# Kernel optimization log

Measured on AMD Instinct MI355X. Metric: run time of the kernel, lower is better.

## Reference

```python
import jax, jax.numpy as jnp
import numpy as np

S, B, D, H = 1024, 8, 256, 8
DH = D // H
N = S * B
E = 262144
EPS = 1e-5


def setup_inputs():
    key = jax.random.key(0)
    ks = jax.random.split(key, 10)
    g = lambda k, shp, s=0.05: jax.random.normal(k, shp, jnp.float32) * s
    return {
        "x": g(ks[0], (S, B, D), 1.0),
        "condition": g(ks[1], (S, B, 1), 1.0),
        "in_proj_w": g(ks[2], (3 * D, D)),
        "in_proj_b": jnp.zeros((3 * D,), jnp.float32),
        "out_proj_w": g(ks[3], (D, D)),
        "out_proj_b": jnp.zeros((D,), jnp.float32),
        "g1": jnp.ones((D,), jnp.float32), "be1": jnp.zeros((D,), jnp.float32),
        "g2": jnp.ones((D,), jnp.float32), "be2": jnp.zeros((D,), jnp.float32),
        "g3": jnp.ones((D,), jnp.float32), "be3": jnp.zeros((D,), jnp.float32),
        "lin_w": g(ks[4], (D, D)),
        "att_src": g(ks[5], (H, DH)),
        "att_dst": g(ks[6], (H, DH)),
        "gat_bias": jnp.zeros((D,), jnp.float32),
        "w1": g(ks[7], (4 * D, D + 1)),
        "bf1": jnp.zeros((4 * D,), jnp.float32),
        "w2": g(ks[8], (D, 4 * D)),
        "bf2": jnp.zeros((D,), jnp.float32),
        "edge_index": jax.random.randint(ks[9], (2, E), 0, N, jnp.int32),
    }


def _ln(x, g, b):
    m = jnp.mean(x, axis=-1, keepdims=True)
    v = jnp.mean((x - m) ** 2, axis=-1, keepdims=True)
    return (x - m) * jax.lax.rsqrt(v + EPS) * g + b


def _forward(x, condition, in_proj_w, in_proj_b, out_proj_w, out_proj_b,
             g1, be1, g2, be2, g3, be3, lin_w, att_src, att_dst, gat_bias,
             w1, bf1, w2, bf2, edge_index):
    # ---- self-attention (torch MHA, seq-major [S,B,D]) ----
    qkv = jnp.einsum('sbd,ed->sbe', x, in_proj_w) + in_proj_b
    q, k, v = jnp.split(qkv, 3, axis=-1)
    q = q.reshape(S, B, H, DH)
    k = k.reshape(S, B, H, DH)
    v = v.reshape(S, B, H, DH)
    scores = jnp.einsum('sbhd,tbhd->bhst', q, k) / np.float32(np.sqrt(DH))
    a = jax.nn.softmax(scores, axis=-1)
    ctx = jnp.einsum('bhst,tbhd->sbhd', a, v).reshape(S, B, D)
    attn_out = ctx @ out_proj_w.T + out_proj_b
    x1 = _ln(x + attn_out, g1, be1)
    # ---- GATConv over flattened (batch-major) nodes ----
    xr = x1.transpose(1, 0, 2).reshape(N, D)          # node i = b*S + s
    xh = (xr @ lin_w.T).reshape(N, H, DH)
    loops = jnp.arange(N, dtype=edge_index.dtype)     # PyG add_self_loops=True
    src = jnp.concatenate([edge_index[0], loops])
    dst = jnp.concatenate([edge_index[1], loops])
    a_src = jnp.sum(xh * att_src, axis=-1)            # [N,H]
    a_dst = jnp.sum(xh * att_dst, axis=-1)
    e = jax.nn.leaky_relu(a_src[src] + a_dst[dst], 0.2)  # [Et,H]
    m = jax.ops.segment_max(e, dst, num_segments=N)
    ee = jnp.exp(e - m[dst])
    z = jax.ops.segment_sum(ee, dst, num_segments=N)
    alpha = ee / z[dst]
    msg = xh[src] * alpha[:, :, None]                 # [Et,H,DH]
    gout = jax.ops.segment_sum(msg, dst, num_segments=N).reshape(N, D) + gat_bias
    gout = gout.reshape(B, S, D).transpose(1, 0, 2)
    x2 = _ln(x1 + gout, g2, be2)
    # ---- conditioned FFN ----
    xc = jnp.concatenate([x2, condition], axis=-1)    # [S,B,D+1]
    h = jax.nn.relu(xc @ w1.T + bf1)
    f = h @ w2.T + bf2
    return _ln(x2 + f, g3, be3)


def reference(x, condition, in_proj_w, in_proj_b, out_proj_w, out_proj_b,
              g1, be1, g2, be2, g3, be3, lin_w, att_src, att_dst, gat_bias,
              w1, bf1, w2, bf2, edge_index):
    return _forward(x, condition, in_proj_w, in_proj_b, out_proj_w, out_proj_b,
                    g1, be1, g2, be2, g3, be3, lin_w, att_src, att_dst, gat_bias,
                    w1, bf1, w2, bf2, edge_index)
```

## Files before the change

### kernel.cpp

```cpp
#include <hip/hip_runtime.h>
#include <hip/hip_bf16.h>

#define S_ 1024
#define B_ 8
#define D_ 256
#define H_ 8
#define DH_ 32
#define N_ 8192
#define E_ 262144
#define ET_ 270336

typedef unsigned short u16;
typedef float f32x4 __attribute__((ext_vector_type(4)));
typedef __bf16 bf16x8 __attribute__((ext_vector_type(8)));
typedef short s16x4 __attribute__((ext_vector_type(4)));

#define QK_SCALE 0.17677669529663687f

__device__ inline u16 f2bf(float v) {
    unsigned int u = __float_as_uint(v);
    u = (u + 0x7fffu + ((u >> 16) & 1u)) >> 16;
    return (u16)u;
}
__device__ inline float bf2f(u16 u) { return __uint_as_float(((unsigned int)u) << 16); }

__device__ inline unsigned int pack_trunc(float lo, float hi) {
    return __builtin_amdgcn_perm(__float_as_uint(hi), __float_as_uint(lo), 0x07060302u);
}

__device__ inline void gload16(const u16* g, u16* l) {
    __builtin_amdgcn_global_load_lds((const __attribute__((address_space(1))) unsigned int*)g,
                                     (__attribute__((address_space(3))) unsigned int*)l, 16, 0, 0);
}

__device__ inline f32x4 mfma16bf(s16x4 a, s16x4 b, f32x4 c) {
#if __has_builtin(__builtin_amdgcn_mfma_f32_16x16x16bf16_1k)
    return __builtin_amdgcn_mfma_f32_16x16x16bf16_1k(a, b, c, 0, 0, 0);
#else
    asm volatile("v_mfma_f32_16x16x16_bf16 %0, %1, %2, %0" : "+v"(c) : "v"(a), "v"(b));
    return c;
#endif
}

__global__ __launch_bounds__(256) void convert_all(const float* __restrict__ x,  const float* __restrict__ wi,
                                                   const float* __restrict__ wo, const float* __restrict__ wl,
                                                   const float* __restrict__ w1, const float* __restrict__ w2,
                                                   u16* __restrict__ Xbf, u16* __restrict__ Wi, u16* __restrict__ Wo,
                                                   u16* __restrict__ Wl, u16* __restrict__ W1, u16* __restrict__ W2,
                                                   int* __restrict__ count, int* __restrict__ cursor)
{
    const int idx = blockIdx.x * 256 + threadIdx.x;
    const int C0 = 524288;
    const int C1 = C0 + 196608;
    const int C2 = C1 + 65536;
    const int C3 = C2 + 65536;
    const int C4 = C3 + 294912;
    const int C5 = C4 + 262144;
    const int C6 = C5 + 16384;
    if (idx < C0) {
        const float4 v = *(const float4*)&x[(size_t)idx * 4];
        u16 o[4] = {f2bf(v.x), f2bf(v.y), f2bf(v.z), f2bf(v.w)};
        *(uint2*)&Xbf[(size_t)idx * 4] = *(uint2*)o;
    }
    else if (idx < C1) { int i = idx - C0; Wi[i] = f2bf(wi[i]); }
    else if (idx < C2) { int i = idx - C1; Wo[i] = f2bf(wo[i]); }
    else if (idx < C3) { int i = idx - C2; Wl[i] = f2bf(wl[i]); }
    else if (idx < C4) { int i = idx - C3; int r = i / 288, k = i - r * 288;
                         W1[i] = (k < 257) ? f2bf(w1[r * 257 + k]) : (u16)0; }
    else if (idx < C5) { int i = idx - C4; W2[i] = f2bf(w2[i]); }
    else if (idx < C6) { int i = idx - C5; if (i < 8192) count[i] = 0; else cursor[i - 8192] = 0; }
}

__global__ __launch_bounds__(256) void gemm_qkv_hist(const u16* __restrict__ A,
                                                     const u16* __restrict__ W,
                                                     const float* __restrict__ bias,
                                                     u16* __restrict__ Cv,
                                                     const int* __restrict__ ei, int* __restrict__ count)
{
    const int tid = threadIdx.x;
    if (blockIdx.x >= 768) {
        const int e = (blockIdx.x - 768) * 256 + tid;
        const int dst = (e < E_) ? ei[E_ + e] : e - E_;
        atomicAdd(&count[dst], 1);
        return;
    }
    __shared__ u16 As[2][128 * 32];
    __shared__ u16 Bs[2][64 * 32];
    const int m0 = (blockIdx.x / 12) * 128, n0 = (blockIdx.x % 12) * 64;
    const int lane = tid & 63, w = tid >> 6;
    const int wm = w >> 1, wn = w & 1;
    const int lr = lane & 15, lg = lane >> 4;

    f32x4 acc[4][2] = {};

    const u16* Ag = A + (size_t)(m0 + (tid >> 2)) * 256 + (tid & 3) * 8;
    const u16* Wg = W + (size_t)(n0 + (tid >> 2)) * 256 + (tid & 3) * 8;

    auto stage = [&](int buf, int k0) {
        gload16(Ag + k0,                    &As[buf][tid * 8]);
        gload16(Ag + (size_t)64 * 256 + k0, &As[buf][64 * 32 + tid * 8]);
        gload16(Wg + k0,                    &Bs[buf][tid * 8]);
    };
    stage(0, 0);
    __syncthreads();
    int cur = 0;
    for (int kt = 0; kt < 8; ++kt) {
        if (kt + 1 < 8) stage(cur ^ 1, (kt + 1) << 5);
        bf16x8 af[4], bg[2];
        #pragma unroll
        for (int i = 0; i < 4; ++i) af[i] = *(const bf16x8*)&As[cur][(wm * 64 + i * 16 + lr) * 32 + lg * 8];
        #pragma unroll
        for (int i = 0; i < 2; ++i) bg[i] = *(const bf16x8*)&Bs[cur][(wn * 32 + i * 16 + lr) * 32 + lg * 8];
        #pragma unroll
        for (int mi = 0; mi < 4; ++mi)
            #pragma unroll
            for (int ni = 0; ni < 2; ++ni)
                acc[mi][ni] = __builtin_amdgcn_mfma_f32_16x16x32_bf16(af[mi], bg[ni], acc[mi][ni], 0, 0, 0);
        __syncthreads();
        cur ^= 1;
    }
    #pragma unroll
    for (int mi = 0; mi < 4; ++mi)
        #pragma unroll
        for (int ni = 0; ni < 2; ++ni) {
            const int col = n0 + wn * 32 + ni * 16 + lr;
            const float bv = bias[col];
            const int part = col >> 8, hh = (col >> 5) & 7, dh = col & 31;
            #pragma unroll
            for (int r = 0; r < 4; ++r) {
                const int row = m0 + wm * 64 + mi * 16 + lg * 4 + r;
                const int ss = row >> 3, bb = row & 7;
                Cv[(((size_t)((part * 8 + bb) * 8 + hh)) * 1024 + ss) * 32 + dh] = f2bf(acc[mi][ni][r] + bv);
            }
        }
}

__global__ __launch_bounds__(512) void attn_mfma(const u16* __restrict__ qkv, u16* __restrict__ ctx,
                                                 const int* __restrict__ count, int* __restrict__ offset)
{
    const int tid = threadIdx.x;
    if (blockIdx.x == 512) {
        __shared__ int s[512];
        const int base = tid * 16;
        int c[16]; int sum = 0;
        #pragma unroll
        for (int i = 0; i < 16; ++i) { c[i] = count[base + i]; sum += c[i]; }
        s[tid] = sum; __syncthreads();
        for (int off = 1; off < 512; off <<= 1) {
            int add = (tid >= off) ? s[tid - off] : 0;
            __syncthreads();
            s[tid] += add;
            __syncthreads();
        }
        int run = (tid == 0) ? 0 : s[tid - 1];
        #pragma unroll
        for (int i = 0; i < 16; ++i) { offset[base + i] = run; run += c[i]; }
        if (tid == 511) offset[8192] = run;
        return;
    }
    const int qt = blockIdx.x & 7, bh = blockIdx.x >> 3;
    const int b = bh >> 3, h = bh & 7;
    const int lane = tid & 63, w = tid >> 6;
    const int c = lane & 15, g = lane >> 4;

    __shared__ __align__(16) u16 Ks[2][128][40];
    __shared__ __align__(16) u16 Vt[2][32][132];

    const size_t plane = (size_t)(b * 8 + h) * 32768;
    const int q0 = qt * 128 + w * 16;
    const bf16x8 qf = *(const bf16x8*)&qkv[plane + (size_t)(q0 + c) * 32 + g * 8];
    const u16* kbase = qkv + 2097152 + plane;

    auto stage = [&](int buf, int kt) {
        const int r = tid >> 2, c0 = (tid & 3) * 8;
        const u16* kp = kbase + (size_t)(kt * 128 + r) * 32 + c0;
        *(uint4*)&Ks[buf][r][c0] = *(const uint4*)kp;
        u16 vb[8];
        *(uint4*)vb = *(const uint4*)(kp + 2097152);
        #pragma unroll
        for (int i = 0; i < 8; ++i) Vt[buf][c0 + i][r] = vb[i];
    };

    float l = 0.f;
    f32x4 o0 = {}, o1 = {};

    stage(0, 0);
    __syncthreads();
    int cur = 0;
    for (int kt = 0; kt < 8; ++kt) {
        if (kt + 1 < 8) stage(cur ^ 1, kt + 1);
        f32x4 sc[8];
        #pragma unroll
        for (int t = 0; t < 8; ++t) {
            const bf16x8 kf = *(const bf16x8*)&Ks[cur][t * 16 + c][g * 8];
            sc[t] = __builtin_amdgcn_mfma_f32_16x16x32_bf16(kf, qf, (f32x4){0.f, 0.f, 0.f, 0.f}, 0, 0, 0);
        }
        unsigned int pb[8][2];
        float ls = 0.f;
        #pragma unroll
        for (int t = 0; t < 8; ++t) {
            const float p0 = __expf(sc[t][0] * QK_SCALE);
            const float p1 = __expf(sc[t][1] * QK_SCALE);
            const float p2 = __expf(sc[t][2] * QK_SCALE);
            const float p3 = __expf(sc[t][3] * QK_SCALE);
            ls += (p0 + p1) + (p2 + p3);
            pb[t][0] = pack_trunc(p0, p1);
            pb[t][1] = pack_trunc(p2, p3);
        }
        l += ls;
        #pragma unroll
        for (int t = 0; t < 8; ++t) {
            union { unsigned int u[2]; s16x4 v; } pu;
            pu.u[0] = pb[t][0]; pu.u[1] = pb[t][1];
            const s16x4 vf0 = *(const s16x4*)&Vt[cur][c][t * 16 + g * 4];
            const s16x4 vf1 = *(const s16x4*)&Vt[cur][16 + c][t * 16 + g * 4];
            o0 = mfma16bf(vf0, pu.v, o0);
            o1 = mfma16bf(vf1, pu.v, o1);
        }
        __syncthreads();
        cur ^= 1;
    }
    l += __shfl_xor(l, 16, 64);
    l += __shfl_xor(l, 32, 64);
    const float inv = 1.f / l;
    u16 ob[8];
    #pragma unroll
    for (int r = 0; r < 4; ++r) { ob[r] = f2bf(o0[r] * inv); ob[4 + r] = f2bf(o1[r] * inv); }
    const size_t obase = ((size_t)(q0 + c) * 8 + b) * 256 + h * 32 + g * 4;
    *(uint2*)&ctx[obase]      = *(uint2*)ob;
    *(uint2*)&ctx[obase + 16] = *(uint2*)(ob + 4);
}

template<int MODE>
__global__ __launch_bounds__(512) void gemm_ln(const u16* __restrict__ A, int lda,
                                               const u16* __restrict__ W, int ldw, int Ksz,
                                               const float* __restrict__ bias,
                                               const float* __restrict__ resid,
                                               const float* __restrict__ gamma,
                                               const float* __restrict__ beta,
                                               const float* __restrict__ att_s,
                                               const float* __restrict__ att_d,
                                               float* __restrict__ outf,
                                               u16* __restrict__ outn,
                                               float* __restrict__ asrc,
                                               float* __restrict__ adst,
                                               const int* __restrict__ ei,
                                               const int* __restrict__ offset,
                                               int* __restrict__ cursor,
                                               int* __restrict__ sorted)
{
    constexpr int BM = 32;
    const int tid = threadIdx.x;
    if (MODE == 0 && blockIdx.x >= 256) {
        const int e = (blockIdx.x - 256) * 512 + tid;
        int src, dst;
        if (e < E_) { src = ei[e]; dst = ei[E_ + e]; }
        else        { src = dst = e - E_; }
        const int pos = offset[dst] + atomicAdd(&cursor[dst], 1);
        sorted[pos] = src;
        return;
    }
    __shared__ u16 As[2][BM * 32];
    __shared__ u16 Bs[2][256 * 32];
    __shared__ float2 red[BM][8];
    const int m0 = blockIdx.x * BM;
    const int lane = tid & 63, w = tid >> 6;
    const int rw = w >> 2, cw = w & 3;
    const int lr = lane & 15, lg = lane >> 4;

    f32x4 acc[4] = {};

    auto stage = [&](int buf, int k0) {
        #pragma unroll
        for (int j = 0; j < 2; ++j) {
            const int idx = tid + j * 512;
            gload16(W + (size_t)(idx >> 2) * ldw + (idx & 3) * 8 + k0, &Bs[buf][idx * 8]);
        }
        if (tid < BM * 4)
            gload16(A + (size_t)(m0 + (tid >> 2)) * lda + (tid & 3) * 8 + k0, &As[buf][tid * 8]);
    };
    stage(0, 0);
    __syncthreads();
    const int nt = Ksz >> 5;
    int cur = 0;
    for (int kt = 0; kt < nt; ++kt) {
        if (kt + 1 < nt) stage(cur ^ 1, (kt + 1) << 5);
        bf16x8 af = *(const bf16x8*)&As[cur][(rw * 16 + lr) * 32 + lg * 8];
        bf16x8 bg[4];
        #pragma unroll
        for (int i = 0; i < 4; ++i)  bg[i] = *(const bf16x8*)&Bs[cur][(cw * 64 + i * 16 + lr) * 32 + lg * 8];
        #pragma unroll
        for (int ni = 0; ni < 4; ++ni)
            acc[ni] = __builtin_amdgcn_mfma_f32_16x16x32_bf16(af, bg[ni], acc[ni], 0, 0, 0);
        __syncthreads();
        cur ^= 1;
    }
    int col[4]; float gam[4], bet[4], bv[4], asv[4], adv[4];
    #pragma unroll
    for (int ni = 0; ni < 4; ++ni) {
        col[ni] = cw * 64 + ni * 16 + lr;
        if (MODE != 1) { gam[ni] = gamma[col[ni]]; bet[ni] = beta[col[ni]]; bv[ni] = bias[col[ni]]; }
        else           { asv[ni] = att_s[col[ni]]; adv[ni] = att_d[col[ni]]; }
    }
    #pragma unroll
    for (int r = 0; r < 4; ++r) {
        const int row = rw * 16 + lg * 4 + r;
        const int grow = m0 + row;
        float s1 = 0.f, s2 = 0.f;
        float2 sp0 = {0.f, 0.f}, sp1 = {0.f, 0.f};
        #pragma unroll
        for (int ni = 0; ni < 4; ++ni) {
            float v = acc[ni][r];
            if (MODE != 1) v += bv[ni] + resid[(size_t)grow * 256 + col[ni]];
            acc[ni][r] = v;
            if (MODE == 1) {
                if (ni < 2) { sp0.x += v * asv[ni]; sp0.y += v * adv[ni]; }
                else        { sp1.x += v * asv[ni]; sp1.y += v * adv[ni]; }
            } else { s1 += v; s2 += v * v; }
        }
        #pragma unroll
        for (int msk = 1; msk < 16; msk <<= 1) {
            if (MODE == 1) {
                sp0.x += __shfl_xor(sp0.x, msk, 64); sp0.y += __shfl_xor(sp0.y, msk, 64);
                sp1.x += __shfl_xor(sp1.x, msk, 64); sp1.y += __shfl_xor(sp1.y, msk, 64);
            } else { s1 += __shfl_xor(s1, msk, 64); s2 += __shfl_xor(s2, msk, 64); }
        }
        if (lr == 0) {
            if (MODE == 1) { red[row][cw * 2] = sp0; red[row][cw * 2 + 1] = sp1; }
            else           { red[row][cw] = (float2){s1, s2}; }
        }
    }
    __syncthreads();
    if (MODE == 1) {
        #pragma unroll
        for (int r = 0; r < 4; ++r) {
            const int grow = m0 + rw * 16 + lg * 4 + r;
            #pragma unroll
            for (int ni = 0; ni < 4; ++ni)
                outn[(size_t)grow * 256 + col[ni]] = f2bf(acc[ni][r]);
        }
        for (int idx = tid; idx < BM * 8; idx += 512) {
            const int row = idx >> 3, h = idx & 7;
            asrc[(size_t)(m0 + row) * 8 + h] = red[row][h].x;
            adst[(size_t)(m0 + row) * 8 + h] = red[row][h].y;
        }
    } else {
        #pragma unroll
        for (int r = 0; r < 4; ++r) {
            const int row = rw * 16 + lg * 4 + r;
            const int grow = m0 + row;
            const float2 t0 = red[row][0], t1 = red[row][1], t2 = red[row][2], t3 = red[row][3];
            const float mean = (t0.x + t1.x + t2.x + t3.x) * (1.f / 256.f);
            const float var  = (t0.y + t1.y + t2.y + t3.y) * (1.f / 256.f) - mean * mean;
            const float rs = rsqrtf(var + 1e-5f);
            #pragma unroll
            for (int ni = 0; ni < 4; ++ni) {
                const float o = (acc[ni][r] - mean) * rs * gam[ni] + bet[ni];
                outf[(size_t)grow * 256 + col[ni]] = o;
                if (MODE == 0) {
                    const int node = (grow & 7) * 1024 + (grow >> 3);
                    outn[(size_t)node * 256 + col[ni]] = f2bf(o);
                }
            }
        }
    }
}

__global__ __launch_bounds__(256) void gat_gather_ln(const int* __restrict__ sorted, const int* __restrict__ offset,
                                                     const float* __restrict__ asrc, const float* __restrict__ adst,
                                                     const u16* __restrict__ xh,
                                                     const float* __restrict__ X1f, const float* __restrict__ gb,
                                                     const float* __restrict__ g2, const float* __restrict__ be2,
                                                     const float* __restrict__ cond,
                                                     float* __restrict__ X2f, u16* __restrict__ X2pad)
{
    const int wid = threadIdx.x >> 6, lane = threadIdx.x & 63;
    const int pair = wid >> 1, half = wid & 1;
    const int dst = blockIdx.x * 2 + pair;
    const int sub = lane >> 5, l32 = lane & 31;
    const int h = l32 >> 2;
    const float ad = adst[dst * 8 + h];
    const int beg = offset[dst], end = offset[dst + 1];
    const int mid = beg + ((end - beg + 1) >> 1);
    const int b0 = half ? mid : beg;
    const int b1 = half ? end : mid;

    __shared__ float szs[2][8];
    __shared__ __align__(16) float sa[2][32][8];

    float z = 0.f;
    float a[8] = {};
    #pragma unroll 2
    for (int i = b0 + sub; i < b1; i += 2) {
        const int src = sorted[i];
        float e = asrc[src * 8 + h] + ad;
        e = fmaxf(e, 0.2f * e);
        const float p = __expf(e);
        z += p;
        const uint4 xv = *(const uint4*)&xh[(size_t)src * 256 + l32 * 8];
        a[0] += p * __uint_as_float(xv.x << 16);
        a[1] += p * __uint_as_float(xv.x & 0xffff0000u);
        a[2] += p * __uint_as_float(xv.y << 16);
        a[3] += p * __uint_as_float(xv.y & 0xffff0000u);
        a[4] += p * __uint_as_float(xv.z << 16);
        a[5] += p * __uint_as_float(xv.z & 0xffff0000u);
        a[6] += p * __uint_as_float(xv.w << 16);
        a[7] += p * __uint_as_float(xv.w & 0xffff0000u);
    }
    z += __shfl_xor(z, 32, 64);
    #pragma unroll
    for (int j = 0; j < 8; ++j) a[j] += __shfl_xor(a[j], 32, 64);
    if (half && sub == 0) {
        if ((l32 & 3) == 0) szs[pair][h] = z;
        *(f32x4*)&sa[pair][l32][0] = (f32x4){a[0], a[1], a[2], a[3]};
        *(f32x4*)&sa[pair][l32][4] = (f32x4){a[4], a[5], a[6], a[7]};
    }
    __syncthreads();
    if (half) return;
    const float zt = z + szs[pair][h];
    const float inv = 1.f / zt;
    const int row = (dst & 1023) * 8 + (dst >> 10);
    float v[8];
    {
        const f32x4 x0 = *(const f32x4*)&X1f[(size_t)row * 256 + l32 * 8];
        const f32x4 x1 = *(const f32x4*)&X1f[(size_t)row * 256 + l32 * 8 + 4];
        const f32x4 gb0 = *(const f32x4*)&gb[l32 * 8];
        const f32x4 gb1 = *(const f32x4*)&gb[l32 * 8 + 4];
        const f32x4 m0 = *(const f32x4*)&sa[pair][l32][0];
        const f32x4 m1 = *(const f32x4*)&sa[pair][l32][4];
        #pragma unroll
        for (int j = 0; j < 4; ++j) {
            v[j]     = x0[j] + (a[j] + m0[j]) * inv + gb0[j];
            v[4 + j] = x1[j] + (a[4 + j] + m1[j]) * inv + gb1[j];
        }
    }
    float s1 = 0.f, s2 = 0.f;
    #pragma unroll
    for (int j = 0; j < 8; ++j) { s1 += v[j]; s2 += v[j] * v[j]; }
    #pragma unroll
    for (int msk = 1; msk < 32; msk <<= 1) { s1 += __shfl_xor(s1, msk, 64); s2 += __shfl_xor(s2, msk, 64); }
    const float mean = s1 * (1.f / 256.f);
    const float var = s2 * (1.f / 256.f) - mean * mean;
    const float rs = rsqrtf(var + 1e-5f);
    if (sub == 0) {
        const f32x4 gg0 = *(const f32x4*)&g2[l32 * 8];
        const f32x4 gg1 = *(const f32x4*)&g2[l32 * 8 + 4];
        const f32x4 be0 = *(const f32x4*)&be2[l32 * 8];
        const f32x4 be1 = *(const f32x4*)&be2[l32 * 8 + 4];
        f32x4 o0, o1;
        u16 ob[8];
        #pragma unroll
        for (int j = 0; j < 4; ++j) {
            o0[j] = (v[j] - mean) * rs * gg0[j] + be0[j];
            o1[j] = (v[4 + j] - mean) * rs * gg1[j] + be1[j];
            ob[j] = f2bf(o0[j]); ob[4 + j] = f2bf(o1[j]);
        }
        *(f32x4*)&X2f[(size_t)row * 256 + l32 * 8]     = o0;
        *(f32x4*)&X2f[(size_t)row * 256 + l32 * 8 + 4] = o1;
        *(uint4*)&X2pad[(size_t)row * 288 + l32 * 8] = *(uint4*)ob;
        if (l32 < 8) {
            u16 zz[4] = {0, 0, 0, 0};
            if (l32 == 0) zz[0] = f2bf(cond[row]);
            *(uint2*)&X2pad[(size_t)row * 288 + 256 + l32 * 4] = *(uint2*)zz;
        }
    }
}

__global__ __launch_bounds__(256) void gemm_w1(const u16* __restrict__ A,
                                               const u16* __restrict__ W,
                                               const float* __restrict__ bias,
                                               u16* __restrict__ Cv)
{
    __shared__ u16 As[2][128 * 32];
    __shared__ u16 Bs[2][128 * 32];
    const int tid = threadIdx.x;
    const int m0 = blockIdx.y * 128, n0 = blockIdx.x * 128;
    const int lane = tid & 63, w = tid >> 6;
    const int wm = w >> 1, wn = w & 1;
    const int lr = lane & 15, lg = lane >> 4;

    f32x4 acc[4][4] = {};

    const u16* Ag = A + (size_t)(m0 + (tid >> 2)) * 288 + (tid & 3) * 8;
    const u16* Wg = W + (size_t)(n0 + (tid >> 2)) * 288 + (tid & 3) * 8;

    auto stage = [&](int buf, int k0) {
        gload16(Ag + k0,                    &As[buf][tid * 8]);
        gload16(Ag + (size_t)64 * 288 + k0, &As[buf][64 * 32 + tid * 8]);
        gload16(Wg + k0,                    &Bs[buf][tid * 8]);
        gload16(Wg + (size_t)64 * 288 + k0, &Bs[buf][64 * 32 + tid * 8]);
    };
    stage(0, 0);
    __syncthreads();
    int cur = 0;
    for (int kt = 0; kt < 9; ++kt) {
        if (kt + 1 < 9) stage(cur ^ 1, (kt + 1) << 5);
        bf16x8 af[4], bg[4];
        #pragma unroll
        for (int i = 0; i < 4; ++i) {
            af[i] = *(const bf16x8*)&As[cur][(wm * 64 + i * 16 + lr) * 32 + lg * 8];
            bg[i] = *(const bf16x8*)&Bs[cur][(wn * 64 + i * 16 + lr) * 32 + lg * 8];
        }
        #pragma unroll
        for (int mi = 0; mi < 4; ++mi)
            #pragma unroll
            for (int ni = 0; ni < 4; ++ni)
                acc[mi][ni] = __builtin_amdgcn_mfma_f32_16x16x32_bf16(af[mi], bg[ni], acc[mi][ni], 0, 0, 0);
        __syncthreads();
        cur ^= 1;
    }
    #pragma unroll
    for (int mi = 0; mi < 4; ++mi)
        #pragma unroll
        for (int ni = 0; ni < 4; ++ni) {
            const int col = n0 + wn * 64 + ni * 16 + lr;
            const float bv = bias[col];
            #pragma unroll
            for (int r = 0; r < 4; ++r) {
                const int row = m0 + wm * 64 + mi * 16 + lg * 4 + r;
                Cv[(size_t)row * 1024 + col] = f2bf(fmaxf(acc[mi][ni][r] + bv, 0.f));
            }
        }
}

extern "C" void kernel_launch(void* const* d_in, const int* in_sizes, int n_in,
                              void* d_out, int out_size, void* d_ws, size_t ws_size,
                              hipStream_t stream)
{
    const float* x          = (const float*)d_in[0];
    const float* condition  = (const float*)d_in[1];
    const float* in_proj_w  = (const float*)d_in[2];
    const float* in_proj_b  = (const float*)d_in[3];
    const float* out_proj_w = (const float*)d_in[4];
    const float* out_proj_b = (const float*)d_in[5];
    const float* g1         = (const float*)d_in[6];
    const float* be1        = (const float*)d_in[7];
    const float* g2         = (const float*)d_in[8];
    const float* be2        = (const float*)d_in[9];
    const float* g3         = (const float*)d_in[10];
    const float* be3        = (const float*)d_in[11];
    const float* lin_w      = (const float*)d_in[12];
    const float* att_src    = (const float*)d_in[13];
    const float* att_dst    = (const float*)d_in[14];
    const float* gat_bias   = (const float*)d_in[15];
    const float* w1         = (const float*)d_in[16];
    const float* bf1        = (const float*)d_in[17];
    const float* w2         = (const float*)d_in[18];
    const float* bf2        = (const float*)d_in[19];
    const int*   edge_index = (const int*)d_in[20];
    float* out = (float*)d_out;

    char* ws = (char*)d_ws;
    u16*   QKV    = (u16*)(ws + 0);
    u16*   Hb     = (u16*)(ws + 0);
    u16*   CTX    = (u16*)(ws + 16777216);
    u16*   X1node = (u16*)(ws + 20971520);
    u16*   XH     = (u16*)(ws + 25165824);
    float* X1f    = (float*)(ws + 29360128);
    float* X2f    = (float*)(ws + 37748736);
    u16*   X2pad  = (u16*)(ws + 46137344);
    u16*   Xbf    = (u16*)(ws + 50855936);
    float* ASRC   = (float*)(ws + 55050240);
    float* ADST   = (float*)(ws + 55312384);
    u16*   W_inp  = (u16*)(ws + 55574528);
    u16*   W_out  = (u16*)(ws + 55967744);
    u16*   W_lin  = (u16*)(ws + 56098816);
    u16*   W_w1   = (u16*)(ws + 56229888);
    u16*   W_w2   = (u16*)(ws + 56819712);
    int*   COUNT  = (int*)(ws + 57344000);
    int*   OFFSET = (int*)(ws + 57376768);
    int*   CURSOR = (int*)(ws + 57413632);
    int*   SORTED = (int*)(ws + 57446400);

    convert_all<<<5568, 256, 0, stream>>>(x, in_proj_w, out_proj_w, lin_w, w1, w2,
                                          Xbf, W_inp, W_out, W_lin, W_w1, W_w2, COUNT, CURSOR);
    gemm_qkv_hist<<<1824, 256, 0, stream>>>(Xbf, W_inp, in_proj_b, QKV, edge_index, COUNT);
    attn_mfma<<<513, 512, 0, stream>>>(QKV, CTX, COUNT, OFFSET);
    gemm_ln<0><<<784, 512, 0, stream>>>(CTX, 256, W_out, 256, 256, out_proj_b, x, g1, be1,
                                        nullptr, nullptr, X1f, X1node, nullptr, nullptr,
                                        edge_index, OFFSET, CURSOR, SORTED);
    gemm_ln<1><<<256, 512, 0, stream>>>(X1node, 256, W_lin, 256, 256, nullptr, nullptr, nullptr, nullptr,
                                        att_src, att_dst, nullptr, XH, ASRC, ADST,
                                        nullptr, nullptr, nullptr, nullptr);
    gat_gather_ln<<<4096, 256, 0, stream>>>(SORTED, OFFSET, ASRC, ADST, XH,
                                            X1f, gat_bias, g2, be2, condition, X2f, X2pad);
    gemm_w1<<<dim3(8, 64), 256, 0, stream>>>(X2pad, W_w1, bf1, Hb);
    gemm_ln<2><<<256, 512, 0, stream>>>(Hb, 1024, W_w2, 1024, 1024, bf2, X2f, g3, be3,
                                        nullptr, nullptr, out, nullptr, nullptr, nullptr,
                                        nullptr, nullptr, nullptr, nullptr);
}
```

Measured before the change: 137.0 us.

## Fuse out-proj+LN1 GEMM with GAT linear projection, keeping X1 tile in LDS

Merges the out-projection+LayerNorm kernel and the GAT lin_w projection kernel into one. Each block keeps its normalized bf16 X1 tile in shared memory and immediately multiplies it by lin_w, scattering XH and attention logits to node-major positions. This removes one kernel launch and the global round-trip of the X1node buffer. In exchange each block uses more LDS, does two GEMM phases serially, and its XH stores are scattered rather than contiguous.

```diff
diff --git a/kernel.cpp b/kernel.cpp
--- a/kernel.cpp
+++ b/kernel.cpp
@@ -231,27 +231,26 @@
     *(uint2*)&ctx[obase + 16] = *(uint2*)(ob + 4);
 }
 
-template<int MODE>
-__global__ __launch_bounds__(512) void gemm_ln(const u16* __restrict__ A, int lda,
-                                               const u16* __restrict__ W, int ldw, int Ksz,
-                                               const float* __restrict__ bias,
-                                               const float* __restrict__ resid,
-                                               const float* __restrict__ gamma,
-                                               const float* __restrict__ beta,
-                                               const float* __restrict__ att_s,
-                                               const float* __restrict__ att_d,
-                                               float* __restrict__ outf,
-                                               u16* __restrict__ outn,
-                                               float* __restrict__ asrc,
-                                               float* __restrict__ adst,
-                                               const int* __restrict__ ei,
-                                               const int* __restrict__ offset,
-                                               int* __restrict__ cursor,
-                                               int* __restrict__ sorted)
-{
-    constexpr int BM = 32;
+__global__ __launch_bounds__(512) void gemm_ln0_xh(const u16* __restrict__ A,
+                                                   const u16* __restrict__ Wo,
+                                                   const u16* __restrict__ Wl,
+                                                   const float* __restrict__ bias,
+                                                   const float* __restrict__ resid,
+                                                   const float* __restrict__ gamma,
+                                                   const float* __restrict__ beta,
+                                                   const float* __restrict__ att_s,
+                                                   const float* __restrict__ att_d,
+                                                   float* __restrict__ X1f,
+                                                   u16* __restrict__ XH,
+                                                   float* __restrict__ asrc,
+                                                   float* __restrict__ adst,
+                                                   const int* __restrict__ ei,
+                                                   const int* __restrict__ offset,
+                                                   int* __restrict__ cursor,
+                                                   int* __restrict__ sorted)
+{
     const int tid = threadIdx.x;
-    if (MODE == 0 && blockIdx.x >= 256) {
+    if (blockIdx.x >= 256) {
         const int e = (blockIdx.x - 256) * 512 + tid;
         int src, dst;
         if (e < E_) { src = ei[e]; dst = ei[E_ + e]; }
@@ -260,6 +259,144 @@
         sorted[pos] = src;
         return;
     }
+    __shared__ u16 As[2][32 * 32];
+    __shared__ u16 Bs[2][256 * 32];
+    __shared__ float2 red[32][8];
+    __shared__ __align__(16) u16 X1s[32][264];
+    const int m0 = blockIdx.x * 32;
+    const int lane = tid & 63, w = tid >> 6;
+    const int rw = w >> 2, cw = w & 3;
+    const int lr = lane & 15, lg = lane >> 4;
+
+    auto stageW = [&](const u16* W, int buf, int k0) {
+        #pragma unroll
+        for (int j = 0; j < 2; ++j) {
+            const int idx = tid + j * 512;
+            gload16(W + (size_t)(idx >> 2) * 256 + (idx & 3) * 8 + k0, &Bs[buf][idx * 8]);
+        }
+    };
+    auto stageA = [&](int buf, int k0) {
+        if (tid < 128)
+            gload16(A + (size_t)(m0 + (tid >> 2)) * 256 + (tid & 3) * 8 + k0, &As[buf][tid * 8]);
+    };
+
+    f32x4 acc[4] = {};
+    stageW(Wo, 0, 0); stageA(0, 0);
+    __syncthreads();
+    int cur = 0;
+    for (int kt = 0; kt < 8; ++kt) {
+        if (kt + 1 < 8) { stageW(Wo, cur ^ 1, (kt + 1) << 5); stageA(cur ^ 1, (kt + 1) << 5); }
+        const bf16x8 af = *(const bf16x8*)&As[cur][(rw * 16 + lr) * 32 + lg * 8];
+        bf16x8 bg[4];
+        #pragma unroll
+        for (int i = 0; i < 4; ++i)  bg[i] = *(const bf16x8*)&Bs[cur][(cw * 64 + i * 16 + lr) * 32 + lg * 8];
+        #pragma unroll
+        for (int ni = 0; ni < 4; ++ni)
+            acc[ni] = __builtin_amdgcn_mfma_f32_16x16x32_bf16(af, bg[ni], acc[ni], 0, 0, 0);
+        __syncthreads();
+        cur ^= 1;
+    }
+    int col[4]; float gam[4], bet[4], bv[4];
+    #pragma unroll
+    for (int ni = 0; ni < 4; ++ni) {
+        col[ni] = cw * 64 + ni * 16 + lr;
+        gam[ni] = gamma[col[ni]]; bet[ni] = beta[col[ni]]; bv[ni] = bias[col[ni]];
+    }
+    #pragma unroll
+    for (int r = 0; r < 4; ++r) {
+        const int row = rw * 16 + lg * 4 + r;
+        const int grow = m0 + row;
+        float s1 = 0.f, s2 = 0.f;
+        #pragma unroll
+        for (int ni = 0; ni < 4; ++ni) {
+            float v = acc[ni][r] + bv[ni] + resid[(size_t)grow * 256 + col[ni]];
+            acc[ni][r] = v;
+            s1 += v; s2 += v * v;
+        }
+        #pragma unroll
+        for (int msk = 1; msk < 16; msk <<= 1) { s1 += __shfl_xor(s1, msk, 64); s2 += __shfl_xor(s2, msk, 64); }
+        if (lr == 0) red[row][cw] = (float2){s1, s2};
+    }
+    __syncthreads();
+    #pragma unroll
+    for (int r = 0; r < 4; ++r) {
+        const int row = rw * 16 + lg * 4 + r;
+        const int grow = m0 + row;
+        const float2 t0 = red[row][0], t1 = red[row][1], t2 = red[row][2], t3 = red[row][3];
+        const float mean = (t0.x + t1.x + t2.x + t3.x) * (1.f / 256.f);
+        const float var  = (t0.y + t1.y + t2.y + t3.y) * (1.f / 256.f) - mean * mean;
+        const float rs = rsqrtf(var + 1e-5f);
+        #pragma unroll
+        for (int ni = 0; ni < 4; ++ni) {
+            const float o = (acc[ni][r] - mean) * rs * gam[ni] + bet[ni];
+            X1f[(size_t)grow * 256 + col[ni]] = o;
+            X1s[row][col[ni]] = f2bf(o);
+        }
+    }
+    f32x4 acc2[4] = {};
+    stageW(Wl, 0, 0);
+    __syncthreads();
+    cur = 0;
+    for (int kt = 0; kt < 8; ++kt) {
+        if (kt + 1 < 8) stageW(Wl, cur ^ 1, (kt + 1) << 5);
+        const bf16x8 af = *(const bf16x8*)&X1s[rw * 16 + lr][kt * 32 + lg * 8];
+        bf16x8 bg[4];
+        #pragma unroll
+        for (int i = 0; i < 4; ++i)  bg[i] = *(const bf16x8*)&Bs[cur][(cw * 64 + i * 16 + lr) * 32 + lg * 8];
+        #pragma unroll
+        for (int ni = 0; ni < 4; ++ni)
+            acc2[ni] = __builtin_amdgcn_mfma_f32_16x16x32_bf16(af, bg[ni], acc2[ni], 0, 0, 0);
+        __syncthreads();
+        cur ^= 1;
+    }
+    float asv[4], adv[4];
+    #pragma unroll
+    for (int ni = 0; ni < 4; ++ni) { asv[ni] = att_s[col[ni]]; adv[ni] = att_d[col[ni]]; }
+    #pragma unroll
+    for (int r = 0; r < 4; ++r) {
+        const int row = rw * 16 + lg * 4 + r;
+        float2 sp0 = {0.f, 0.f}, sp1 = {0.f, 0.f};
+        #pragma unroll
+        for (int ni = 0; ni < 4; ++ni) {
+            const float v = acc2[ni][r];
+            if (ni < 2) { sp0.x += v * asv[ni]; sp0.y += v * adv[ni]; }
+            else        { sp1.x += v * asv[ni]; sp1.y += v * adv[ni]; }
+        }
+        #pragma unroll
+        for (int msk = 1; msk < 16; msk <<= 1) {
+            sp0.x += __shfl_xor(sp0.x, msk, 64); sp0.y += __shfl_xor(sp0.y, msk, 64);
+            sp1.x += __shfl_xor(sp1.x, msk, 64); sp1.y += __shfl_xor(sp1.y, msk, 64);
+        }
+        if (lr == 0) { red[row][cw * 2] = sp0; red[row][cw * 2 + 1] = sp1; }
+    }
+    __syncthreads();
+    #pragma unroll
+    for (int r = 0; r < 4; ++r) {
+        const int grow = m0 + rw * 16 + lg * 4 + r;
+        const int node = (grow & 7) * 1024 + (grow >> 3);
+        #pragma unroll
+        for (int ni = 0; ni < 4; ++ni)
+            XH[(size_t)node * 256 + col[ni]] = f2bf(acc2[ni][r]);
+    }
+    for (int idx = tid; idx < 32 * 8; idx += 512) {
+        const int row = idx >> 3, h = idx & 7;
+        const int grow = m0 + row;
+        const int node = (grow & 7) * 1024 + (grow >> 3);
+        asrc[(size_t)node * 8 + h] = red[row][h].x;
+        adst[(size_t)node * 8 + h] = red[row][h].y;
+    }
+}
+
+__global__ __launch_bounds__(512) void gemm_ln2(const u16* __restrict__ A, int lda,
+                                                const u16* __restrict__ W, int ldw, int Ksz,
+                                                const float* __restrict__ bias,
+                                                const float* __restrict__ resid,
+                                                const float* __restrict__ gamma,
+                                                const float* __restrict__ beta,
+                                                float* __restrict__ outf)
+{
+    constexpr int BM = 32;
+    const int tid = threadIdx.x;
     __shared__ u16 As[2][BM * 32];
     __shared__ u16 Bs[2][256 * 32];
     __shared__ float2 red[BM][8];
@@ -295,74 +432,39 @@
         __syncthreads();
         cur ^= 1;
     }
-    int col[4]; float gam[4], bet[4], bv[4], asv[4], adv[4];
+    int col[4]; float gam[4], bet[4], bv[4];
     #pragma unroll
     for (int ni = 0; ni < 4; ++ni) {
         col[ni] = cw * 64 + ni * 16 + lr;
-        if (MODE != 1) { gam[ni] = gamma[col[ni]]; bet[ni] = beta[col[ni]]; bv[ni] = bias[col[ni]]; }
-        else           { asv[ni] = att_s[col[ni]]; adv[ni] = att_d[col[ni]]; }
+        gam[ni] = gamma[col[ni]]; bet[ni] = beta[col[ni]]; bv[ni] = bias[col[ni]];
     }
     #pragma unroll
     for (int r = 0; r < 4; ++r) {
         const int row = rw * 16 + lg * 4 + r;
         const int grow = m0 + row;
         float s1 = 0.f, s2 = 0.f;
-        float2 sp0 = {0.f, 0.f}, sp1 = {0.f, 0.f};
         #pragma unroll
         for (int ni = 0; ni < 4; ++ni) {
-            float v = acc[ni][r];
-            if (MODE != 1) v += bv[ni] + resid[(size_t)grow * 256 + col[ni]];
+            float v = acc[ni][r] + bv[ni] + resid[(size_t)grow * 256 + col[ni]];
             acc[ni][r] = v;
-            if (MODE == 1) {
-                if (ni < 2) { sp0.x += v * asv[ni]; sp0.y += v * adv[ni]; }
-                else        { sp1.x += v * asv[ni]; sp1.y += v * adv[ni]; }
-            } else { s1 += v; s2 += v * v; }
-        }
-        #pragma unroll
-        for (int msk = 1; msk < 16; msk <<= 1) {
-            if (MODE == 1) {
-                sp0.x += __shfl_xor(sp0.x, msk, 64); sp0.y += __shfl_xor(sp0.y, msk, 64);
-                sp1.x += __shfl_xor(sp1.x, msk, 64); sp1.y += __shfl_xor(sp1.y, msk, 64);
-            } else { s1 += __shfl_xor(s1, msk, 64); s2 += __shfl_xor(s2, msk, 64); }
-        }
-        if (lr == 0) {
-            if (MODE == 1) { red[row][cw * 2] = sp0; red[row][cw * 2 + 1] = sp1; }
-            else           { red[row][cw] = (float2){s1, s2}; }
-        }
-    }
-    __syncthreads();
-    if (MODE == 1) {
-        #pragma unroll
-        for (int r = 0; r < 4; ++r) {
-            const int grow = m0 + rw * 16 + lg * 4 + r;
-            #pragma unroll
-            for (int ni = 0; ni < 4; ++ni)
-                outn[(size_t)grow * 256 + col[ni]] = f2bf(acc[ni][r]);
-        }
-        for (int idx = tid; idx < BM * 8; idx += 512) {
-            const int row = idx >> 3, h = idx & 7;
-            asrc[(size_t)(m0 + row) * 8 + h] = red[row][h].x;
-            adst[(size_t)(m0 + row) * 8 + h] = red[row][h].y;
-        }
-    } else {
-        #pragma unroll
-        for (int r = 0; r < 4; ++r) {
-            const int row = rw * 16 + lg * 4 + r;
-            const int grow = m0 + row;
-            const float2 t0 = red[row][0], t1 = red[row][1], t2 = red[row][2], t3 = red[row][3];
-            const float mean = (t0.x + t1.x + t2.x + t3.x) * (1.f / 256.f);
-            const float var  = (t0.y + t1.y + t2.y + t3.y) * (1.f / 256.f) - mean * mean;
-            const float rs = rsqrtf(var + 1e-5f);
-            #pragma unroll
-            for (int ni = 0; ni < 4; ++ni) {
-                const float o = (acc[ni][r] - mean) * rs * gam[ni] + bet[ni];
-                outf[(size_t)grow * 256 + col[ni]] = o;
-                if (MODE == 0) {
-                    const int node = (grow & 7) * 1024 + (grow >> 3);
-                    outn[(size_t)node * 256 + col[ni]] = f2bf(o);
-                }
-            }
-        }
+            s1 += v; s2 += v * v;
+        }
+        #pragma unroll
+        for (int msk = 1; msk < 16; msk <<= 1) { s1 += __shfl_xor(s1, msk, 64); s2 += __shfl_xor(s2, msk, 64); }
+        if (lr == 0) red[row][cw] = (float2){s1, s2};
+    }
+    __syncthreads();
+    #pragma unroll
+    for (int r = 0; r < 4; ++r) {
+        const int row = rw * 16 + lg * 4 + r;
+        const int grow = m0 + row;
+        const float2 t0 = red[row][0], t1 = red[row][1], t2 = red[row][2], t3 = red[row][3];
+        const float mean = (t0.x + t1.x + t2.x + t3.x) * (1.f / 256.f);
+        const float var  = (t0.y + t1.y + t2.y + t3.y) * (1.f / 256.f) - mean * mean;
+        const float rs = rsqrtf(var + 1e-5f);
+        #pragma unroll
+        for (int ni = 0; ni < 4; ++ni)
+            outf[(size_t)grow * 256 + col[ni]] = (acc[ni][r] - mean) * rs * gam[ni] + bet[ni];
     }
 }
 
@@ -554,7 +656,6 @@
     u16*   QKV    = (u16*)(ws + 0);
     u16*   Hb     = (u16*)(ws + 0);
     u16*   CTX    = (u16*)(ws + 16777216);
-    u16*   X1node = (u16*)(ws + 20971520);
     u16*   XH     = (u16*)(ws + 25165824);
     float* X1f    = (float*)(ws + 29360128);
     float* X2f    = (float*)(ws + 37748736);
@@ -576,16 +677,11 @@
                                           Xbf, W_inp, W_out, W_lin, W_w1, W_w2, COUNT, CURSOR);
     gemm_qkv_hist<<<1824, 256, 0, stream>>>(Xbf, W_inp, in_proj_b, QKV, edge_index, COUNT);
     attn_mfma<<<513, 512, 0, stream>>>(QKV, CTX, COUNT, OFFSET);
-    gemm_ln<0><<<784, 512, 0, stream>>>(CTX, 256, W_out, 256, 256, out_proj_b, x, g1, be1,
-                                        nullptr, nullptr, X1f, X1node, nullptr, nullptr,
-                                        edge_index, OFFSET, CURSOR, SORTED);
-    gemm_ln<1><<<256, 512, 0, stream>>>(X1node, 256, W_lin, 256, 256, nullptr, nullptr, nullptr, nullptr,
-                                        att_src, att_dst, nullptr, XH, ASRC, ADST,
-                                        nullptr, nullptr, nullptr, nullptr);
+    gemm_ln0_xh<<<784, 512, 0, stream>>>(CTX, W_out, W_lin, out_proj_b, x, g1, be1,
+                                         att_src, att_dst, X1f, XH, ASRC, ADST,
+                                         edge_index, OFFSET, CURSOR, SORTED);
     gat_gather_ln<<<4096, 256, 0, stream>>>(SORTED, OFFSET, ASRC, ADST, XH,
                                             X1f, gat_bias, g2, be2, condition, X2f, X2pad);
     gemm_w1<<<dim3(8, 64), 256, 0, stream>>>(X2pad, W_w1, bf1, Hb);
-    gemm_ln<2><<<256, 512, 0, stream>>>(Hb, 1024, W_w2, 1024, 1024, bf2, X2f, g3, be3,
-                                        nullptr, nullptr, out, nullptr, nullptr, nullptr,
-                                        nullptr, nullptr, nullptr, nullptr);
-}
+    gemm_ln2<<<256, 512, 0, stream>>>(Hb, 1024, W_w2, 1024, 1024, bf2, X2f, g3, be3, out);
+}
```

Result: faster. 133.8 us (-2.3%).
